# Kernel optimization log

Hardware: AMD Instinct MI355X
Metric: run time of the kernel (lower is better)

Reference implementation:

```python
import jax, jax.numpy as jnp
import numpy as np

D_MODEL = 512
N_EXPERTS = 8
TOP_K = 2
B, S = 2, 4096


def setup_inputs() -> dict:
    key = jax.random.key(0)
    ks = jax.random.split(key, 8)
    d, h, e = D_MODEL, 4 * D_MODEL, N_EXPERTS
    sc_in = 1.0 / np.sqrt(d)
    sc_h = 1.0 / np.sqrt(h)
    return {
        "x": jax.random.normal(ks[0], (B, S, d), dtype=jnp.float32),
        "time_stage": jax.random.normal(ks[1], (B, S, d), dtype=jnp.float32),
        "gate_w": jax.random.normal(ks[2], (d, e), dtype=jnp.float32) * sc_in,
        "gate_b": jnp.zeros((e,), dtype=jnp.float32),
        "w1": jax.random.normal(ks[3], (e, d, h), dtype=jnp.float32) * sc_in,
        "b1": jnp.zeros((e, h), dtype=jnp.float32),
        "w2": jax.random.normal(ks[4], (e, h, d), dtype=jnp.float32) * sc_h,
        "b2": jnp.zeros((e, d), dtype=jnp.float32),
    }


def reference(x, time_stage, gate_w, gate_b, w1, b1, w2, b2):
    # Router: softmax over experts of gate(x + stop_grad(TimeStage))
    router_input = x + jax.lax.stop_gradient(time_stage)
    gate_score = jax.nn.softmax(router_input @ gate_w + gate_b, axis=-1)  # [B,S,E]
    topk_val, topk_idx = jax.lax.top_k(gate_score, TOP_K)  # [B,S,K]

    # Per-token per-expert combine weight: sum of top-k probs routed to expert e
    # (zero for non-selected experts) -> [B,S,E]
    onehot = jax.nn.one_hot(topk_idx, N_EXPERTS, dtype=x.dtype)  # [B,S,K,E]
    weights = jnp.einsum("bske,bsk->bse", onehot, topk_val)

    # Dense grouped expert MLP; tokens with zero weight contribute nothing,
    # matching the original masked gather/scatter loop exactly.
    h = jax.nn.gelu(jnp.einsum("bsd,edf->ebsf", x, w1) + b1[:, None, None, :],
                    approximate=False)  # [E,B,S,4D]
    y = jnp.einsum("ebsf,efd->ebsd", h, w2) + b2[:, None, None, :]  # [E,B,S,D]
    out = jnp.einsum("bse,ebsd->bsd", weights, y)
    return out
```

## Files before the change

kernel.cpp:

```cpp
#include <hip/hip_runtime.h>
#include <math.h>

#define D 512
#define H 2048
#define E 8
#define NTOK 8192
#define BK 64
#define PTMAX 17408

typedef __attribute__((ext_vector_type(8))) short bf16x8;
typedef __attribute__((ext_vector_type(4))) float f32x4;

__device__ __forceinline__ short f2b(float v) {
    unsigned u = __float_as_uint(v);
    unsigned r = (u + 0x7FFFu + ((u >> 16) & 1u)) >> 16;
    return (short)r;
}
__device__ __forceinline__ float b2f(short v) {
    unsigned u = ((unsigned)(unsigned short)v) << 16;
    return __uint_as_float(u);
}
__device__ __forceinline__ float gelu_exact(float v) {
    return 0.5f * v * (1.0f + erff(v * 0.70710678118654752f));
}
__device__ __forceinline__ float gelu_fast(float v) {
    float u2 = -1.5957691216f * (v + 0.044715f * v * v * v);
    return v / (1.f + __expf(u2));
}
__device__ __forceinline__ void gll16(const void* g, void* l) {
    __builtin_amdgcn_global_load_lds(
        (const __attribute__((address_space(1))) void*)g,
        (__attribute__((address_space(3))) void*)l, 16, 0, 0);
}
__device__ __forceinline__ void seg_of(const int* cnt, int e, int& s0, int& P) {
    int o = 0;
#pragma unroll
    for (int i = 0; i < E; ++i) {
        int p = (cnt[i] + 127) & ~127;
        if (i < e) o += p;
        if (i == e) P = p;
    }
    s0 = o;
}

__global__ __launch_bounds__(256) void router_score(
    const float* __restrict__ x, const float* __restrict__ ts,
    const float* __restrict__ gw, const float* __restrict__ gb,
    int* __restrict__ sel, float2* __restrict__ wsel,
    short* __restrict__ xbf)
{
    int wave = threadIdx.x >> 6, lane = threadIdx.x & 63;
    int t = blockIdx.x * 4 + wave;

    const float* xr = x + (size_t)t * D + lane * 8;
    const float* tr = ts + (size_t)t * D + lane * 8;
    float4 xa = *reinterpret_cast<const float4*>(xr);
    float4 xb = *reinterpret_cast<const float4*>(xr + 4);
    float4 ta = *reinterpret_cast<const float4*>(tr);
    float4 tb = *reinterpret_cast<const float4*>(tr + 4);

    bf16x8 o;
    o[0] = f2b(xa.x); o[1] = f2b(xa.y); o[2] = f2b(xa.z); o[3] = f2b(xa.w);
    o[4] = f2b(xb.x); o[5] = f2b(xb.y); o[6] = f2b(xb.z); o[7] = f2b(xb.w);
    *reinterpret_cast<bf16x8*>(xbf + (size_t)t * D + lane * 8) = o;

    float v[8] = {xa.x + ta.x, xa.y + ta.y, xa.z + ta.z, xa.w + ta.w,
                  xb.x + tb.x, xb.y + tb.y, xb.z + tb.z, xb.w + tb.w};
    float acc[E];
#pragma unroll
    for (int e2 = 0; e2 < E; ++e2) acc[e2] = 0.f;
#pragma unroll
    for (int i = 0; i < 8; ++i) {
        const float4* gr = reinterpret_cast<const float4*>(gw + (size_t)(lane * 8 + i) * E);
        float4 g0 = gr[0], g1 = gr[1];
        acc[0] += v[i] * g0.x; acc[1] += v[i] * g0.y; acc[2] += v[i] * g0.z; acc[3] += v[i] * g0.w;
        acc[4] += v[i] * g1.x; acc[5] += v[i] * g1.y; acc[6] += v[i] * g1.z; acc[7] += v[i] * g1.w;
    }
#pragma unroll
    for (int m = 32; m; m >>= 1) {
#pragma unroll
        for (int e2 = 0; e2 < E; ++e2) acc[e2] += __shfl_xor(acc[e2], m);
    }
    if (lane == 0) {
        float p[E]; float mx;
#pragma unroll
        for (int e2 = 0; e2 < E; ++e2) p[e2] = acc[e2] + gb[e2];
        mx = p[0];
#pragma unroll
        for (int e2 = 1; e2 < E; ++e2) mx = fmaxf(mx, p[e2]);
        float s = 0.f;
#pragma unroll
        for (int e2 = 0; e2 < E; ++e2) { p[e2] = expf(p[e2] - mx); s += p[e2]; }
        float inv = 1.f / s;
        int i0 = 0; float v0 = p[0];
#pragma unroll
        for (int e2 = 1; e2 < E; ++e2) if (p[e2] > v0) { v0 = p[e2]; i0 = e2; }
        int i1 = (i0 == 0) ? 1 : 0; float v1 = p[i1];
#pragma unroll
        for (int e2 = 0; e2 < E; ++e2)
            if (e2 != i0 && e2 != ((i0 == 0) ? 1 : 0) && p[e2] > v1) { v1 = p[e2]; i1 = e2; }
        sel[t]  = i0 | (i1 << 8);
        wsel[t] = make_float2(v0 * inv, v1 * inv);
    }
}

__global__ __launch_bounds__(256) void scatter_tokens(
    const int* __restrict__ sel, const float2* __restrict__ wsel,
    int* __restrict__ cnt, int* __restrict__ tok_id, float* __restrict__ tok_w)
{
    __shared__ int lh[E];
    __shared__ int gbase[E];
    int tid = threadIdx.x;
    int t = blockIdx.x * 256 + tid;
    if (tid < E) lh[tid] = 0;
    __syncthreads();
    int s = sel[t];
    float2 w = wsel[t];
    int e0 = s & 255, e1 = s >> 8;
    int p0 = atomicAdd(&lh[e0], 1);
    int p1 = atomicAdd(&lh[e1], 1);
    __syncthreads();
    if (tid < E) gbase[tid] = atomicAdd(&cnt[tid], lh[tid]);
    __syncthreads();
    int o0 = gbase[e0] + p0;
    int o1 = gbase[e1] + p1;
    tok_id[e0 * NTOK + o0] = t;
    tok_w [e0 * NTOK + o0] = w.x;
    tok_id[e1 * NTOK + o1] = t;
    tok_w [e1 * NTOK + o1] = w.y;
}

__global__ __launch_bounds__(256) void router_kernel(
    const float* __restrict__ x, const float* __restrict__ ts,
    const float* __restrict__ gw, const float* __restrict__ gb,
    int* __restrict__ cnt, int* __restrict__ tok_id, float* __restrict__ tok_w)
{
    int t = blockIdx.x * blockDim.x + threadIdx.x;
    if (t >= NTOK) return;
    float acc[E];
#pragma unroll
    for (int e = 0; e < E; ++e) acc[e] = gb[e];
    const float* xr = x + (size_t)t * D;
    const float* tr = ts + (size_t)t * D;
#pragma unroll 4
    for (int d = 0; d < D; ++d) {
        float xv = xr[d] + tr[d];
        const float4* g4 = reinterpret_cast<const float4*>(gw + d * E);
        float4 a = g4[0], b = g4[1];
        acc[0] += xv * a.x; acc[1] += xv * a.y; acc[2] += xv * a.z; acc[3] += xv * a.w;
        acc[4] += xv * b.x; acc[5] += xv * b.y; acc[6] += xv * b.z; acc[7] += xv * b.w;
    }
    float m = acc[0];
#pragma unroll
    for (int e = 1; e < E; ++e) m = fmaxf(m, acc[e]);
    float p[E]; float s = 0.f;
#pragma unroll
    for (int e = 0; e < E; ++e) { p[e] = expf(acc[e] - m); s += p[e]; }
    float inv = 1.f / s;
    int i0 = 0; float v0 = p[0];
#pragma unroll
    for (int e = 1; e < E; ++e) if (p[e] > v0) { v0 = p[e]; i0 = e; }
    int i1 = (i0 == 0) ? 1 : 0; float v1 = p[i1];
#pragma unroll
    for (int e = 0; e < E; ++e) if (e != i0 && e != ((i0 == 0) ? 1 : 0) && p[e] > v1) { v1 = p[e]; i1 = e; }
    int pos0 = atomicAdd(&cnt[i0], 1);
    tok_id[i0 * NTOK + pos0] = t;
    tok_w[i0 * NTOK + pos0] = v0 * inv;
    int pos1 = atomicAdd(&cnt[i1], 1);
    tok_id[i1 * NTOK + pos1] = t;
    tok_w[i1 * NTOK + pos1] = v1 * inv;
}

__global__ __launch_bounds__(256) void pad_fill(
    const int* __restrict__ cnt, const int* __restrict__ sel,
    const int* __restrict__ tok_id, const float* __restrict__ tok_w,
    int* __restrict__ pad_tok, float* __restrict__ pad_w, int* __restrict__ inv)
{
    int e = blockIdx.y;
    int i = blockIdx.x * 256 + threadIdx.x;
    int s, P;
    seg_of(cnt, e, s, P);
    if (i < P) {
        int n = cnt[e];
        int tok = (i < n) ? tok_id[e * NTOK + i] : 0;
        pad_tok[s + i] = tok;
        pad_w[s + i]   = (i < n) ? tok_w[e * NTOK + i] : 0.f;
        if (i < n) {
            int k = ((sel[tok] & 255) == e) ? 0 : 1;
            inv[tok * 2 + k] = s + i;
        }
    }
}

__global__ __launch_bounds__(256) void transpose_cvt2(
    const float* __restrict__ w1, short* __restrict__ w1t,
    const float* __restrict__ w2, short* __restrict__ w2t)
{
    int z = blockIdx.z;
    const float* src; short* dst; int R, C, rt, ct;
    if (z < E) {
        src = w1 + (size_t)z * D * H; dst = w1t + (size_t)z * D * H;
        R = D; C = H; rt = blockIdx.x * 64; ct = blockIdx.y * 64;
    } else {
        src = w2 + (size_t)(z - E) * H * D; dst = w2t + (size_t)(z - E) * H * D;
        R = H; C = D; rt = blockIdx.y * 64; ct = blockIdx.x * 64;
    }
    __shared__ float tsb[64][68];
    int tid = threadIdx.x;
    int r  = tid >> 4;
    int c4 = (tid & 15) * 4;
    for (int rr = r; rr < 64; rr += 16) {
        float4 v = *reinterpret_cast<const float4*>(src + (size_t)(rt + rr) * C + ct + c4);
        tsb[rr][c4] = v.x; tsb[rr][c4 + 1] = v.y; tsb[rr][c4 + 2] = v.z; tsb[rr][c4 + 3] = v.w;
    }
    __syncthreads();
    for (int cr = r; cr < 64; cr += 16) {
        short4 o;
        o.x = f2b(tsb[c4 + 0][cr]);
        o.y = f2b(tsb[c4 + 1][cr]);
        o.z = f2b(tsb[c4 + 2][cr]);
        o.w = f2b(tsb[c4 + 3][cr]);
        *reinterpret_cast<short4*>(dst + (size_t)(ct + cr) * R + rt + c4) = o;
    }
}

__global__ __launch_bounds__(256, 2) void gemm1(
    const short* __restrict__ xbf,
    const short* __restrict__ w1t, const float* __restrict__ b1,
    const int* __restrict__ cnt, const int* __restrict__ pad_tok,
    short* __restrict__ hbuf)
{
    int bid = blockIdx.x;
    int e  = bid & 7;
    int u  = bid >> 3;
    int nt = u & 15;
    int mt = u >> 4;
    int s0, P;
    seg_of(cnt, e, s0, P);
    if (mt * 128 >= P) return;
    int p0 = s0 + mt * 128;

    __shared__ short As[2][128 * BK];
    __shared__ short Bs[2][128 * BK];

    int tid = threadIdx.x;
    int wv = tid >> 6, lane = tid & 63;
    int q = lane >> 4, r = lane & 15;
    int wm = wv >> 1, wn = wv & 1;

    const short* w1e = w1t + (size_t)e * H * D;

    const short* asrc[4];
    const short* bsrc[4];
#pragma unroll
    for (int p = 0; p < 4; ++p) {
        int g = p * 256 + tid;
        int row = g >> 3;
        int slot = (g & 7) ^ (row & 7);
        int tok = pad_tok[p0 + row];
        asrc[p] = xbf + (size_t)tok * D + slot * 8;
        bsrc[p] = w1e + (size_t)(nt * 128 + row) * D + slot * 8;
    }

    f32x4 acc[4][4];
#pragma unroll
    for (int m = 0; m < 4; ++m)
#pragma unroll
        for (int n = 0; n < 4; ++n) acc[m][n] = (f32x4){0.f, 0.f, 0.f, 0.f};

    const int xorv = r & 7;

#pragma unroll
    for (int p = 0; p < 4; ++p) {
        gll16(asrc[p], &As[0][p * 2048 + wv * 512]);
        gll16(bsrc[p], &Bs[0][p * 2048 + wv * 512]);
    }

    const int NTT = D / BK;
    for (int t = 0; t < NTT; ++t) {
        int b = t & 1;
        if (t + 1 < NTT) {
            int kk = (t + 1) * BK;
#pragma unroll
            for (int p = 0; p < 4; ++p) {
                gll16(asrc[p] + kk, &As[b ^ 1][p * 2048 + wv * 512]);
                gll16(bsrc[p] + kk, &Bs[b ^ 1][p * 2048 + wv * 512]);
            }
            asm volatile("s_waitcnt vmcnt(8)" ::: "memory");
        } else {
            asm volatile("s_waitcnt vmcnt(0)" ::: "memory");
        }
        __builtin_amdgcn_s_barrier();
        __builtin_amdgcn_sched_barrier(0);

        const char* Ab = (const char*)&As[b][0];
        const char* Bb = (const char*)&Bs[b][0];
#pragma unroll
        for (int ks = 0; ks < 2; ++ks) {
            int sslot = ((ks * 4 + q) ^ xorv) << 4;
            bf16x8 a[4], bb[4];
#pragma unroll
            for (int m = 0; m < 4; ++m)
                a[m] = *(const bf16x8*)(Ab + (wm * 64 + m * 16 + r) * 128 + sslot);
#pragma unroll
            for (int n = 0; n < 4; ++n)
                bb[n] = *(const bf16x8*)(Bb + (wn * 64 + n * 16 + r) * 128 + sslot);
            __builtin_amdgcn_s_setprio(1);
#pragma unroll
            for (int m = 0; m < 4; ++m)
#pragma unroll
                for (int n = 0; n < 4; ++n)
                    acc[m][n] = __builtin_amdgcn_mfma_f32_16x16x32_bf16(a[m], bb[n], acc[m][n], 0, 0, 0);
            __builtin_amdgcn_s_setprio(0);
        }
        if (t + 1 < NTT) {
            __builtin_amdgcn_s_barrier();
            __builtin_amdgcn_sched_barrier(0);
        }
    }
    __syncthreads();

    const float* b1e = b1 + (size_t)e * H;
    float bv[4];
#pragma unroll
    for (int n = 0; n < 4; ++n) bv[n] = b1e[nt * 128 + wn * 64 + n * 16 + r];
    short* slab = &As[0][0];
#pragma unroll
    for (int m = 0; m < 4; ++m)
#pragma unroll
        for (int j = 0; j < 4; ++j) {
            int lr = wm * 64 + m * 16 + q * 4 + j;
#pragma unroll
            for (int n = 0; n < 4; ++n) {
                int col = wn * 64 + n * 16 + r;
                slab[lr * 128 + col] = f2b(gelu_fast(acc[m][n][j] + bv[n]));
            }
        }
    __syncthreads();
#pragma unroll
    for (int p = 0; p < 8; ++p) {
        int idx = p * 256 + tid;
        int row = idx >> 4;
        int c16 = idx & 15;
        bf16x8 v = *reinterpret_cast<const bf16x8*>(&slab[row * 128 + c16 * 8]);
        *reinterpret_cast<bf16x8*>(&hbuf[(size_t)(p0 + row) * H + nt * 128 + c16 * 8]) = v;
    }
}

__global__ __launch_bounds__(256, 2) void gemm2(
    const short* __restrict__ hbuf,
    const short* __restrict__ w2t, const float* __restrict__ b2,
    const int* __restrict__ cnt,
    short* __restrict__ ybuf)
{
    int bid = blockIdx.x;
    int e  = bid & 7;
    int u  = bid >> 3;
    int nt = u & 3;
    int mt = u >> 2;
    int s0, P;
    seg_of(cnt, e, s0, P);
    if (mt * 128 >= P) return;
    int p0 = s0 + mt * 128;

    __shared__ short As[2][128 * BK];
    __shared__ short Bs[2][128 * BK];

    int tid = threadIdx.x;
    int wv = tid >> 6, lane = tid & 63;
    int q = lane >> 4, r = lane & 15;
    int wm = wv >> 1, wn = wv & 1;

    const short* w2e = w2t + (size_t)e * D * H;

    const short* asrc[4];
    const short* bsrc[4];
#pragma unroll
    for (int p = 0; p < 4; ++p) {
        int g = p * 256 + tid;
        int row = g >> 3;
        int slot = (g & 7) ^ (row & 7);
        asrc[p] = hbuf + (size_t)(p0 + row) * H + slot * 8;
        bsrc[p] = w2e + (size_t)(nt * 128 + row) * H + slot * 8;
    }

    f32x4 acc[4][4];
#pragma unroll
    for (int m = 0; m < 4; ++m)
#pragma unroll
        for (int n = 0; n < 4; ++n) acc[m][n] = (f32x4){0.f, 0.f, 0.f, 0.f};

    const int xorv = r & 7;

#pragma unroll
    for (int p = 0; p < 4; ++p) {
        gll16(asrc[p], &As[0][p * 2048 + wv * 512]);
        gll16(bsrc[p], &Bs[0][p * 2048 + wv * 512]);
    }

    const int NTT = H / BK;
    for (int t = 0; t < NTT; ++t) {
        int b = t & 1;
        if (t + 1 < NTT) {
            int kk = (t + 1) * BK;
#pragma unroll
            for (int p = 0; p < 4; ++p) {
                gll16(asrc[p] + kk, &As[b ^ 1][p * 2048 + wv * 512]);
                gll16(bsrc[p] + kk, &Bs[b ^ 1][p * 2048 + wv * 512]);
            }
            asm volatile("s_waitcnt vmcnt(8)" ::: "memory");
        } else {
            asm volatile("s_waitcnt vmcnt(0)" ::: "memory");
        }
        __builtin_amdgcn_s_barrier();
        __builtin_amdgcn_sched_barrier(0);

        const char* Ab = (const char*)&As[b][0];
        const char* Bb = (const char*)&Bs[b][0];
#pragma unroll
        for (int ks = 0; ks < 2; ++ks) {
            int sslot = ((ks * 4 + q) ^ xorv) << 4;
            bf16x8 a[4], bb[4];
#pragma unroll
            for (int m = 0; m < 4; ++m)
                a[m] = *(const bf16x8*)(Ab + (wm * 64 + m * 16 + r) * 128 + sslot);
#pragma unroll
            for (int n = 0; n < 4; ++n)
                bb[n] = *(const bf16x8*)(Bb + (wn * 64 + n * 16 + r) * 128 + sslot);
            __builtin_amdgcn_s_setprio(1);
#pragma unroll
            for (int m = 0; m < 4; ++m)
#pragma unroll
                for (int n = 0; n < 4; ++n)
                    acc[m][n] = __builtin_amdgcn_mfma_f32_16x16x32_bf16(a[m], bb[n], acc[m][n], 0, 0, 0);
            __builtin_amdgcn_s_setprio(0);
        }
        if (t + 1 < NTT) {
            __builtin_amdgcn_s_barrier();
            __builtin_amdgcn_sched_barrier(0);
        }
    }
    __syncthreads();

    const float* b2e = b2 + (size_t)e * D;
    float bv[4];
#pragma unroll
    for (int n = 0; n < 4; ++n) bv[n] = b2e[nt * 128 + wn * 64 + n * 16 + r];
    short* slab = &As[0][0];
#pragma unroll
    for (int m = 0; m < 4; ++m)
#pragma unroll
        for (int j = 0; j < 4; ++j) {
            int lr = wm * 64 + m * 16 + q * 4 + j;
#pragma unroll
            for (int n = 0; n < 4; ++n) {
                int col = wn * 64 + n * 16 + r;
                slab[lr * 128 + col] = f2b(acc[m][n][j] + bv[n]);
            }
        }
    __syncthreads();
#pragma unroll
    for (int p = 0; p < 8; ++p) {
        int idx = p * 256 + tid;
        int row = idx >> 4;
        int c16 = idx & 15;
        bf16x8 v = *reinterpret_cast<const bf16x8*>(&slab[row * 128 + c16 * 8]);
        *reinterpret_cast<bf16x8*>(&ybuf[(size_t)(p0 + row) * D + nt * 128 + c16 * 8]) = v;
    }
}

__global__ __launch_bounds__(256) void combine(
    const short* __restrict__ ybuf, const int* __restrict__ inv,
    const float2* __restrict__ wsel, float* __restrict__ out)
{
    int gid = blockIdx.x * 256 + threadIdx.x;
    int t  = gid >> 7;
    int c4 = (gid & 127) * 4;
    float2 w = wsel[t];
    int i0 = inv[t * 2], i1 = inv[t * 2 + 1];
    short4 y0 = *reinterpret_cast<const short4*>(ybuf + (size_t)i0 * D + c4);
    short4 y1 = *reinterpret_cast<const short4*>(ybuf + (size_t)i1 * D + c4);
    float4 o;
    o.x = w.x * b2f(y0.x) + w.y * b2f(y1.x);
    o.y = w.x * b2f(y0.y) + w.y * b2f(y1.y);
    o.z = w.x * b2f(y0.z) + w.y * b2f(y1.z);
    o.w = w.x * b2f(y0.w) + w.y * b2f(y1.w);
    *reinterpret_cast<float4*>(out + (size_t)t * D + c4) = o;
}

#define TMM 64
#define FCC 64
#define XPAD 520
#define HPD 72

__global__ __launch_bounds__(512, 2) void ffn_mfma(
    const float* __restrict__ x,
    const short* __restrict__ w1t, const float* __restrict__ b1,
    const short* __restrict__ w2t, const float* __restrict__ b2,
    const int* __restrict__ cnt, const int* __restrict__ tok_id,
    const float* __restrict__ tok_w,
    float* __restrict__ out)
{
    int b = blockIdx.x;
    int e = b & 7;
    int tile = b >> 3;
    int n = cnt[e];
    int start = tile * TMM;
    if (start >= n) return;
    int nvalid = min(TMM, n - start);

    __shared__ short xs[TMM * XPAD];
    __shared__ short hs[TMM * HPD];
    __shared__ int   stok[TMM];
    __shared__ float sw[TMM];

    int tid = threadIdx.x;
    if (tid < TMM) {
        int tok = 0; float w = 0.f;
        if (tid < nvalid) {
            tok = tok_id[e * NTOK + start + tid];
            w   = tok_w[e * NTOK + start + tid];
        }
        stok[tid] = tok; sw[tid] = w;
    }
    __syncthreads();

    for (int idx = tid; idx < TMM * (D / 4); idx += 512) {
        int row = idx >> 7;
        int c4  = (idx & 127) << 2;
        float4 v = *reinterpret_cast<const float4*>(x + (size_t)stok[row] * D + c4);
        short4 o; o.x = f2b(v.x); o.y = f2b(v.y); o.z = f2b(v.z); o.w = f2b(v.w);
        *reinterpret_cast<short4*>(&xs[row * XPAD + c4]) = o;
    }
    __syncthreads();

    const int lane = tid & 63, wave = tid >> 6;
    const int wm = wave >> 2, wn = wave & 3;
    const int q = lane >> 4,  r = lane & 15;

    const short* w1e = w1t + (size_t)e * H * D;
    const short* w2e = w2t + (size_t)e * D * H;
    const float* b1e = b1 + (size_t)e * H;
    const float* b2e = b2 + (size_t)e * D;

    f32x4 acc[2][8];
#pragma unroll
    for (int i = 0; i < 2; ++i)
#pragma unroll
        for (int j = 0; j < 8; ++j) acc[i][j] = (f32x4){0.f, 0.f, 0.f, 0.f};

    for (int fc = 0; fc < H; fc += FCC) {
        int f = fc + wn * 16 + r;
        float b1f = b1e[f];
        f32x4 h0 = {b1f, b1f, b1f, b1f};
        f32x4 h1 = h0;
        const short* wrow = w1e + (size_t)f * D;
        const short* a0p = &xs[(wm * 32 + r) * XPAD + q * 8];
        const short* a1p = a0p + 16 * XPAD;
#pragma unroll
        for (int ks = 0; ks < 16; ++ks) {
            bf16x8 bfr = *reinterpret_cast<const bf16x8*>(wrow + ks * 32 + q * 8);
            bf16x8 a0  = *reinterpret_cast<const bf16x8*>(a0p + ks * 32);
            bf16x8 a1  = *reinterpret_cast<const bf16x8*>(a1p + ks * 32);
            h0 = __builtin_amdgcn_mfma_f32_16x16x32_bf16(a0, bfr, h0, 0, 0, 0);
            h1 = __builtin_amdgcn_mfma_f32_16x16x32_bf16(a1, bfr, h1, 0, 0, 0);
        }
        {
            int c = wn * 16 + r;
#pragma unroll
            for (int j = 0; j < 4; ++j) {
                hs[(wm * 32 + q * 4 + j) * HPD + c]      = f2b(gelu_exact(h0[j]));
                hs[(wm * 32 + 16 + q * 4 + j) * HPD + c] = f2b(gelu_exact(h1[j]));
            }
        }
        __syncthreads();
#pragma unroll
        for (int ks = 0; ks < 2; ++ks) {
            bf16x8 a20 = *reinterpret_cast<const bf16x8*>(&hs[(wm * 32 + r) * HPD + ks * 32 + q * 8]);
            bf16x8 a21 = *reinterpret_cast<const bf16x8*>(&hs[(wm * 32 + 16 + r) * HPD + ks * 32 + q * 8]);
#pragma unroll
            for (int nr = 0; nr < 8; ++nr) {
                int dout = wn * 128 + nr * 16 + r;
                bf16x8 bfr = *reinterpret_cast<const bf16x8*>(
                    w2e + (size_t)dout * H + fc + ks * 32 + q * 8);
                acc[0][nr] = __builtin_amdgcn_mfma_f32_16x16x32_bf16(a20, bfr, acc[0][nr], 0, 0, 0);
                acc[1][nr] = __builtin_amdgcn_mfma_f32_16x16x32_bf16(a21, bfr, acc[1][nr], 0, 0, 0);
            }
        }
        __syncthreads();
    }

#pragma unroll
    for (int mrep = 0; mrep < 2; ++mrep) {
#pragma unroll
        for (int j = 0; j < 4; ++j) {
            int rl = wm * 32 + mrep * 16 + q * 4 + j;
            if (rl < nvalid) {
                float w = sw[rl];
                if (w != 0.f) {
                    float* orow = out + (size_t)stok[rl] * D;
#pragma unroll
                    for (int nr = 0; nr < 8; ++nr) {
                        int dout = wn * 128 + nr * 16 + r;
                        f32x4 a = acc[mrep][nr];
                        atomicAdd(&orow[dout], w * (a[j] + b2e[dout]));
                    }
                }
            }
        }
    }
}

extern "C" void kernel_launch(void* const* d_in, const int* in_sizes, int n_in,
                              void* d_out, int out_size, void* d_ws, size_t ws_size,
                              hipStream_t stream) {
    const float* x  = (const float*)d_in[0];
    const float* ts = (const float*)d_in[1];
    const float* gw = (const float*)d_in[2];
    const float* gb = (const float*)d_in[3];
    const float* w1 = (const float*)d_in[4];
    const float* b1 = (const float*)d_in[5];
    const float* w2 = (const float*)d_in[6];
    const float* b2 = (const float*)d_in[7];
    float* out = (float*)d_out;

    int*    cnt     = (int*)d_ws;
    int*    tok_id  = (int*)((char*)d_ws + 1024);
    float*  tok_w   = (float*)((char*)d_ws + 263168);
    int*    pad_tok = (int*)((char*)d_ws + 525312);
    float*  pad_w   = (float*)((char*)d_ws + 594944);
    int*    sel     = (int*)((char*)d_ws + 665600);
    float2* wsel    = (float2*)((char*)d_ws + 700416);
    int*    inv     = (int*)((char*)d_ws + 765952);
    short*  xbf     = (short*)((char*)d_ws + 1048576);
    short*  w1t     = (short*)((char*)d_ws + 9437184);
    short*  w2t     = (short*)((char*)d_ws + 26214400);
    short*  hbuf    = (short*)((char*)d_ws + 42991616);
    short*  ybuf    = (short*)((char*)d_ws + 1048576);
    const size_t ws_need = 114294784;

    hipMemsetAsync(cnt, 0, 64, stream);

    if (ws_size >= ws_need) {
        router_score<<<NTOK / 4, 256, 0, stream>>>(x, ts, gw, gb, sel, wsel, xbf);
        scatter_tokens<<<NTOK / 256, 256, 0, stream>>>(sel, wsel, cnt, tok_id, tok_w);
        pad_fill<<<dim3(NTOK / 256, E), 256, 0, stream>>>(cnt, sel, tok_id, tok_w,
                                                          pad_tok, pad_w, inv);
        transpose_cvt2<<<dim3(8, 32, 2 * E), 256, 0, stream>>>(w1, w1t, w2, w2t);
        gemm1<<<E * 64 * 16, 256, 0, stream>>>(xbf, w1t, b1, cnt, pad_tok, hbuf);
        gemm2<<<E * 64 * 4, 256, 0, stream>>>(hbuf, w2t, b2, cnt, ybuf);
        combine<<<NTOK * (D / 4) / 256, 256, 0, stream>>>(ybuf, inv, wsel, out);
    } else {
        hipMemsetAsync(out, 0, (size_t)out_size * sizeof(float), stream);
        short* w1t_f = (short*)((char*)d_ws + (1u << 20));
        short* w2t_f = w1t_f + (size_t)E * D * H;
        router_kernel<<<NTOK / 256, 256, 0, stream>>>(x, ts, gw, gb, cnt, tok_id, tok_w);
        transpose_cvt2<<<dim3(8, 32, 2 * E), 256, 0, stream>>>(w1, w1t_f, w2, w2t_f);
        ffn_mfma<<<(NTOK / TMM) * E, 512, 0, stream>>>(
            x, w1t_f, b1, w2t_f, b2, cnt, tok_id, tok_w, out);
    }
}
```

Before: 190.4 us.

## Shrink GEMM K-tile to 32, halve gemm2 M-tile, raise occupancy

Both expert GEMMs drop from a 64-wide K tile with an XOR-swizzled LDS layout to a 32-wide K tile stored slot-major (k-chunk then row), which cuts LDS per block so four blocks can share a CU. gemm2 also halves its M tile to 64 rows and doubles its grid, giving finer load balance over the padded expert segments. The aim is more latency hiding through occupancy. The cost is twice as many barrier-synchronised K iterations, possible LDS bank conflicts now that the swizzle is gone, and less operand reuse per block in gemm2.

```diff
diff --git a/kernel.cpp b/kernel.cpp
--- a/kernel.cpp
+++ b/kernel.cpp
@@ -5,7 +5,6 @@
 #define H 2048
 #define E 8
 #define NTOK 8192
-#define BK 64
 #define PTMAX 17408
 
 typedef __attribute__((ext_vector_type(8))) short bf16x8;
@@ -224,7 +223,7 @@
     }
 }
 
-__global__ __launch_bounds__(256, 2) void gemm1(
+__global__ __launch_bounds__(256, 4) void gemm1(
     const short* __restrict__ xbf,
     const short* __restrict__ w1t, const float* __restrict__ b1,
     const int* __restrict__ cnt, const int* __restrict__ pad_tok,
@@ -240,8 +239,7 @@
     if (mt * 128 >= P) return;
     int p0 = s0 + mt * 128;
 
-    __shared__ short As[2][128 * BK];
-    __shared__ short Bs[2][128 * BK];
+    __shared__ short lds[16384];
 
     int tid = threadIdx.x;
     int wv = tid >> 6, lane = tid & 63;
@@ -250,13 +248,12 @@
 
     const short* w1e = w1t + (size_t)e * H * D;
 
-    const short* asrc[4];
-    const short* bsrc[4];
-#pragma unroll
-    for (int p = 0; p < 4; ++p) {
+    const short* asrc[2];
+    const short* bsrc[2];
+#pragma unroll
+    for (int p = 0; p < 2; ++p) {
         int g = p * 256 + tid;
-        int row = g >> 3;
-        int slot = (g & 7) ^ (row & 7);
+        int slot = g >> 7, row = g & 127;
         int tok = pad_tok[p0 + row];
         asrc[p] = xbf + (size_t)tok * D + slot * 8;
         bsrc[p] = w1e + (size_t)(nt * 128 + row) * D + slot * 8;
@@ -268,51 +265,45 @@
 #pragma unroll
         for (int n = 0; n < 4; ++n) acc[m][n] = (f32x4){0.f, 0.f, 0.f, 0.f};
 
-    const int xorv = r & 7;
-
-#pragma unroll
-    for (int p = 0; p < 4; ++p) {
-        gll16(asrc[p], &As[0][p * 2048 + wv * 512]);
-        gll16(bsrc[p], &Bs[0][p * 2048 + wv * 512]);
-    }
-
-    const int NTT = D / BK;
+#pragma unroll
+    for (int p = 0; p < 2; ++p) {
+        gll16(asrc[p], &lds[p * 2048 + wv * 512]);
+        gll16(bsrc[p], &lds[8192 + p * 2048 + wv * 512]);
+    }
+
+    const int NTT = D / 32;
     for (int t = 0; t < NTT; ++t) {
         int b = t & 1;
         if (t + 1 < NTT) {
-            int kk = (t + 1) * BK;
-#pragma unroll
-            for (int p = 0; p < 4; ++p) {
-                gll16(asrc[p] + kk, &As[b ^ 1][p * 2048 + wv * 512]);
-                gll16(bsrc[p] + kk, &Bs[b ^ 1][p * 2048 + wv * 512]);
+            int kk = (t + 1) * 32;
+#pragma unroll
+            for (int p = 0; p < 2; ++p) {
+                gll16(asrc[p] + kk, &lds[(b ^ 1) * 4096 + p * 2048 + wv * 512]);
+                gll16(bsrc[p] + kk, &lds[8192 + (b ^ 1) * 4096 + p * 2048 + wv * 512]);
             }
-            asm volatile("s_waitcnt vmcnt(8)" ::: "memory");
+            asm volatile("s_waitcnt vmcnt(4)" ::: "memory");
         } else {
             asm volatile("s_waitcnt vmcnt(0)" ::: "memory");
         }
         __builtin_amdgcn_s_barrier();
         __builtin_amdgcn_sched_barrier(0);
 
-        const char* Ab = (const char*)&As[b][0];
-        const char* Bb = (const char*)&Bs[b][0];
-#pragma unroll
-        for (int ks = 0; ks < 2; ++ks) {
-            int sslot = ((ks * 4 + q) ^ xorv) << 4;
-            bf16x8 a[4], bb[4];
-#pragma unroll
-            for (int m = 0; m < 4; ++m)
-                a[m] = *(const bf16x8*)(Ab + (wm * 64 + m * 16 + r) * 128 + sslot);
+        const short* Ab = &lds[b * 4096];
+        const short* Bb = &lds[8192 + b * 4096];
+        bf16x8 a[4], bb[4];
+#pragma unroll
+        for (int m = 0; m < 4; ++m)
+            a[m] = *reinterpret_cast<const bf16x8*>(Ab + q * 1024 + (wm * 64 + m * 16 + r) * 8);
+#pragma unroll
+        for (int n = 0; n < 4; ++n)
+            bb[n] = *reinterpret_cast<const bf16x8*>(Bb + q * 1024 + (wn * 64 + n * 16 + r) * 8);
+        __builtin_amdgcn_s_setprio(1);
+#pragma unroll
+        for (int m = 0; m < 4; ++m)
 #pragma unroll
             for (int n = 0; n < 4; ++n)
-                bb[n] = *(const bf16x8*)(Bb + (wn * 64 + n * 16 + r) * 128 + sslot);
-            __builtin_amdgcn_s_setprio(1);
-#pragma unroll
-            for (int m = 0; m < 4; ++m)
-#pragma unroll
-                for (int n = 0; n < 4; ++n)
-                    acc[m][n] = __builtin_amdgcn_mfma_f32_16x16x32_bf16(a[m], bb[n], acc[m][n], 0, 0, 0);
-            __builtin_amdgcn_s_setprio(0);
-        }
+                acc[m][n] = __builtin_amdgcn_mfma_f32_16x16x32_bf16(a[m], bb[n], acc[m][n], 0, 0, 0);
+        __builtin_amdgcn_s_setprio(0);
         if (t + 1 < NTT) {
             __builtin_amdgcn_s_barrier();
             __builtin_amdgcn_sched_barrier(0);
@@ -324,7 +315,6 @@
     float bv[4];
 #pragma unroll
     for (int n = 0; n < 4; ++n) bv[n] = b1e[nt * 128 + wn * 64 + n * 16 + r];
-    short* slab = &As[0][0];
 #pragma unroll
     for (int m = 0; m < 4; ++m)
 #pragma unroll
@@ -333,7 +323,7 @@
 #pragma unroll
             for (int n = 0; n < 4; ++n) {
                 int col = wn * 64 + n * 16 + r;
-                slab[lr * 128 + col] = f2b(gelu_fast(acc[m][n][j] + bv[n]));
+                lds[lr * 128 + col] = f2b(gelu_fast(acc[m][n][j] + bv[n]));
             }
         }
     __syncthreads();
@@ -342,12 +332,12 @@
         int idx = p * 256 + tid;
         int row = idx >> 4;
         int c16 = idx & 15;
-        bf16x8 v = *reinterpret_cast<const bf16x8*>(&slab[row * 128 + c16 * 8]);
+        bf16x8 v = *reinterpret_cast<const bf16x8*>(&lds[row * 128 + c16 * 8]);
         *reinterpret_cast<bf16x8*>(&hbuf[(size_t)(p0 + row) * H + nt * 128 + c16 * 8]) = v;
     }
 }
 
-__global__ __launch_bounds__(256, 2) void gemm2(
+__global__ __launch_bounds__(256, 4) void gemm2(
     const short* __restrict__ hbuf,
     const short* __restrict__ w2t, const float* __restrict__ b2,
     const int* __restrict__ cnt,
@@ -360,11 +350,10 @@
     int mt = u >> 2;
     int s0, P;
     seg_of(cnt, e, s0, P);
-    if (mt * 128 >= P) return;
-    int p0 = s0 + mt * 128;
-
-    __shared__ short As[2][128 * BK];
-    __shared__ short Bs[2][128 * BK];
+    if (mt * 64 >= P) return;
+    int p0 = s0 + mt * 64;
+
+    __shared__ short lds[12288];
 
     int tid = threadIdx.x;
     int wv = tid >> 6, lane = tid & 63;
@@ -373,68 +362,62 @@
 
     const short* w2e = w2t + (size_t)e * D * H;
 
-    const short* asrc[4];
-    const short* bsrc[4];
-#pragma unroll
-    for (int p = 0; p < 4; ++p) {
+    const short* asrc;
+    {
+        int slot = tid >> 6, row = tid & 63;
+        asrc = hbuf + (size_t)(p0 + row) * H + slot * 8;
+    }
+    const short* bsrc[2];
+#pragma unroll
+    for (int p = 0; p < 2; ++p) {
         int g = p * 256 + tid;
-        int row = g >> 3;
-        int slot = (g & 7) ^ (row & 7);
-        asrc[p] = hbuf + (size_t)(p0 + row) * H + slot * 8;
+        int slot = g >> 7, row = g & 127;
         bsrc[p] = w2e + (size_t)(nt * 128 + row) * H + slot * 8;
     }
 
-    f32x4 acc[4][4];
-#pragma unroll
-    for (int m = 0; m < 4; ++m)
+    f32x4 acc[2][4];
+#pragma unroll
+    for (int m = 0; m < 2; ++m)
 #pragma unroll
         for (int n = 0; n < 4; ++n) acc[m][n] = (f32x4){0.f, 0.f, 0.f, 0.f};
 
-    const int xorv = r & 7;
-
-#pragma unroll
-    for (int p = 0; p < 4; ++p) {
-        gll16(asrc[p], &As[0][p * 2048 + wv * 512]);
-        gll16(bsrc[p], &Bs[0][p * 2048 + wv * 512]);
-    }
-
-    const int NTT = H / BK;
+    gll16(asrc, &lds[wv * 512]);
+#pragma unroll
+    for (int p = 0; p < 2; ++p)
+        gll16(bsrc[p], &lds[4096 + p * 2048 + wv * 512]);
+
+    const int NTT = H / 32;
     for (int t = 0; t < NTT; ++t) {
         int b = t & 1;
         if (t + 1 < NTT) {
-            int kk = (t + 1) * BK;
-#pragma unroll
-            for (int p = 0; p < 4; ++p) {
-                gll16(asrc[p] + kk, &As[b ^ 1][p * 2048 + wv * 512]);
-                gll16(bsrc[p] + kk, &Bs[b ^ 1][p * 2048 + wv * 512]);
-            }
-            asm volatile("s_waitcnt vmcnt(8)" ::: "memory");
+            int kk = (t + 1) * 32;
+            gll16(asrc + kk, &lds[(b ^ 1) * 2048 + wv * 512]);
+#pragma unroll
+            for (int p = 0; p < 2; ++p)
+                gll16(bsrc[p] + kk, &lds[4096 + (b ^ 1) * 4096 + p * 2048 + wv * 512]);
+            asm volatile("s_waitcnt vmcnt(3)" ::: "memory");
         } else {
             asm volatile("s_waitcnt vmcnt(0)" ::: "memory");
         }
         __builtin_amdgcn_s_barrier();
         __builtin_amdgcn_sched_barrier(0);
 
-        const char* Ab = (const char*)&As[b][0];
-        const char* Bb = (const char*)&Bs[b][0];
-#pragma unroll
-        for (int ks = 0; ks < 2; ++ks) {
-            int sslot = ((ks * 4 + q) ^ xorv) << 4;
-            bf16x8 a[4], bb[4];
-#pragma unroll
-            for (int m = 0; m < 4; ++m)
-                a[m] = *(const bf16x8*)(Ab + (wm * 64 + m * 16 + r) * 128 + sslot);
+        const short* Ab = &lds[b * 2048];
+        const short* Bb = &lds[4096 + b * 4096];
+        bf16x8 a[2], bb[4];
+#pragma unroll
+        for (int m = 0; m < 2; ++m)
+            a[m] = *reinterpret_cast<const bf16x8*>(Ab + q * 512 + (wm * 32 + m * 16 + r) * 8);
+#pragma unroll
+        for (int n = 0; n < 4; ++n)
+            bb[n] = *reinterpret_cast<const bf16x8*>(Bb + q * 1024 + (wn * 64 + n * 16 + r) * 8);
+        __builtin_amdgcn_s_setprio(1);
+#pragma unroll
+        for (int m = 0; m < 2; ++m)
 #pragma unroll
             for (int n = 0; n < 4; ++n)
-                bb[n] = *(const bf16x8*)(Bb + (wn * 64 + n * 16 + r) * 128 + sslot);
-            __builtin_amdgcn_s_setprio(1);
-#pragma unroll
-            for (int m = 0; m < 4; ++m)
-#pragma unroll
-                for (int n = 0; n < 4; ++n)
-                    acc[m][n] = __builtin_amdgcn_mfma_f32_16x16x32_bf16(a[m], bb[n], acc[m][n], 0, 0, 0);
-            __builtin_amdgcn_s_setprio(0);
-        }
+                acc[m][n] = __builtin_amdgcn_mfma_f32_16x16x32_bf16(a[m], bb[n], acc[m][n], 0, 0, 0);
+        __builtin_amdgcn_s_setprio(0);
         if (t + 1 < NTT) {
             __builtin_amdgcn_s_barrier();
             __builtin_amdgcn_sched_barrier(0);
@@ -446,25 +429,24 @@
     float bv[4];
 #pragma unroll
     for (int n = 0; n < 4; ++n) bv[n] = b2e[nt * 128 + wn * 64 + n * 16 + r];
-    short* slab = &As[0][0];
-#pragma unroll
-    for (int m = 0; m < 4; ++m)
+#pragma unroll
+    for (int m = 0; m < 2; ++m)
 #pragma unroll
         for (int j = 0; j < 4; ++j) {
-            int lr = wm * 64 + m * 16 + q * 4 + j;
+            int lr = wm * 32 + m * 16 + q * 4 + j;
 #pragma unroll
             for (int n = 0; n < 4; ++n) {
                 int col = wn * 64 + n * 16 + r;
-                slab[lr * 128 + col] = f2b(acc[m][n][j] + bv[n]);
+                lds[lr * 128 + col] = f2b(acc[m][n][j] + bv[n]);
             }
         }
     __syncthreads();
 #pragma unroll
-    for (int p = 0; p < 8; ++p) {
+    for (int p = 0; p < 4; ++p) {
         int idx = p * 256 + tid;
         int row = idx >> 4;
         int c16 = idx & 15;
-        bf16x8 v = *reinterpret_cast<const bf16x8*>(&slab[row * 128 + c16 * 8]);
+        bf16x8 v = *reinterpret_cast<const bf16x8*>(&lds[row * 128 + c16 * 8]);
         *reinterpret_cast<bf16x8*>(&ybuf[(size_t)(p0 + row) * D + nt * 128 + c16 * 8]) = v;
     }
 }
@@ -647,8 +629,8 @@
         pad_fill<<<dim3(NTOK / 256, E), 256, 0, stream>>>(cnt, sel, tok_id, tok_w,
                                                           pad_tok, pad_w, inv);
         transpose_cvt2<<<dim3(8, 32, 2 * E), 256, 0, stream>>>(w1, w1t, w2, w2t);
-        gemm1<<<E * 64 * 16, 256, 0, stream>>>(xbf, w1t, b1, cnt, pad_tok, hbuf);
-        gemm2<<<E * 64 * 4, 256, 0, stream>>>(hbuf, w2t, b2, cnt, ybuf);
+        gemm1<<<E * 16 * 64, 256, 0, stream>>>(xbf, w1t, b1, cnt, pad_tok, hbuf);
+        gemm2<<<E * 4 * 128, 256, 0, stream>>>(hbuf, w2t, b2, cnt, ybuf);
         combine<<<NTOK * (D / 4) / 256, 256, 0, stream>>>(ybuf, inv, wsel, out);
     } else {
         hipMemsetAsync(out, 0, (size_t)out_size * sizeof(float), stream);
```

After: 261.1 us. +37.1%, slower.
